# Kernel tuning notes

Hardware: AMD Instinct MI355X
Metric: run time of the kernel (lower is better)

The kernel has to match this reference:

```python
import jax, jax.numpy as jnp
import numpy as np

N, K, VF, FILT, H = 100000, 10, 128, 64, 3


def setup_inputs() -> dict:
    key = jax.random.key(0)
    ks = jax.random.split(key, 16)
    scale_w = float(np.sqrt(2.0 / VF))
    scale_a = float(np.sqrt(2.0 / (2 * FILT)))

    def pad_idx(k1, k2):
        idx = jax.random.randint(k1, (N, K), 0, N, dtype=jnp.int32)
        drop = jax.random.uniform(k2, (N, K)) < 0.2
        return jnp.where(drop, jnp.int32(-1), idx)

    return {
        "vertices_int": jax.random.normal(ks[0], (N, VF), jnp.float32),
        "vertices_nh": jax.random.normal(ks[1], (N, VF), jnp.float32),
        "nh_indices": pad_idx(ks[2], ks[3]),
        "int_indices": pad_idx(ks[4], ks[5]),
        "nh_edges": jax.random.uniform(ks[6], (N, K), jnp.float32),
        "int_edges": jax.random.uniform(ks[7], (N, K), jnp.float32),
        "is_int": jax.random.randint(ks[8], (N, 1), 0, 2, dtype=jnp.int32),
        "Wvc_int": jax.random.normal(ks[9], (H, VF, FILT), jnp.float32) * scale_w,
        "Wvc_nh": jax.random.normal(ks[10], (H, VF, FILT), jnp.float32) * scale_w,
        "Wvn_int": jax.random.normal(ks[11], (H, VF, FILT), jnp.float32) * scale_w,
        "Wvn_nh": jax.random.normal(ks[12], (H, VF, FILT), jnp.float32) * scale_w,
        "bv_int": jnp.zeros((H, FILT), jnp.float32),
        "bv_nh": jnp.zeros((H, FILT), jnp.float32),
        "a_int": jax.random.normal(ks[13], (H, 2 * FILT, 1), jnp.float32) * scale_a,
        "a_nh": jax.random.normal(ks[14], (H, 2 * FILT, 1), jnp.float32) * scale_a,
    }


def _gat_branch(v, idx, edges, Wvc, Wvn, a, bv):
    # v: [N,VF]; idx,edges: [N,K]; Wvc/Wvn: [H,VF,F]; a: [H,2F,1]; bv: [H,F]
    F_ = Wvc.shape[-1]
    Zc = jnp.einsum('nf,hfo->hno', v, Wvc)        # [H,N,F]
    Zn_src = jnp.einsum('nf,hfo->hno', v, Wvn)     # [H,N,F]
    gath = Zn_src[:, idx]                          # [H,N,K,F]  (-1 wraps, masked below)
    a1, a2 = a[:, :F_, 0], a[:, F_:, 0]            # [H,F] each
    part = (idx != -1).astype(v.dtype)             # [N,K]
    e = (jnp.einsum('hnkf,hf->hnk', gath, a1)
         + jnp.einsum('hnf,hf->hn', Zc, a2)[:, :, None]) * part * edges  # [H,N,K]
    alpha = jax.nn.softmax(e, axis=2)              # softmax over neighbor axis (torch dim=1)
    norm = jnp.maximum(part.sum(axis=1), 1.0)      # [N], zeros clamped to 1
    Zn = jnp.einsum('hnkf,hnk,nk->hnf', gath, alpha, part) / norm[None, :, None]
    z = jax.nn.relu(Zc + Zn + bv[:, None, :])      # [H,N,F]
    n = v.shape[0]
    return jnp.transpose(z, (1, 0, 2)).reshape(n, -1)  # concat heads -> [N, H*F]


def reference(vertices_int, vertices_nh, nh_indices, int_indices, nh_edges,
              int_edges, is_int, Wvc_int, Wvc_nh, Wvn_int, Wvn_nh,
              bv_int, bv_nh, a_int, a_nh):
    v_int = vertices_int * (is_int == 1).astype(vertices_int.dtype)
    v_nh = vertices_nh * (is_int == 0).astype(vertices_nh.dtype)
    out_int = _gat_branch(v_int, int_indices, int_edges, Wvc_int, Wvn_int, a_int, bv_int)
    out_nh = _gat_branch(v_nh, nh_indices, nh_edges, Wvc_nh, Wvn_nh, a_nh, bv_nh)
    return out_int, out_nh
```

## Files before the change

### kernel.cpp

```cpp
#include <hip/hip_runtime.h>


#define NN   100000
#define VFD  128
#define FILT 64
#define NH   3
#define KK   10
#define OUTC 192
#define NB   ((NN + 63) / 64)

typedef __attribute__((ext_vector_type(8))) short  short8;
typedef __attribute__((ext_vector_type(4))) float  f32x4;
typedef __attribute__((ext_vector_type(8))) __bf16 bf16x8;
typedef unsigned int u32;
typedef unsigned short u16;

static __device__ __forceinline__ f32x4 mfma_bf16(short8 a, short8 b, f32x4 c) {
    return __builtin_amdgcn_mfma_f32_16x16x32_bf16(
        __builtin_bit_cast(bf16x8, a), __builtin_bit_cast(bf16x8, b), c, 0, 0, 0);
}

static __device__ __forceinline__ void split2(float x, u16 &hi, u16 &lo) {
    u32 b = __float_as_uint(x);
    hi = (u16)(b >> 16);
    float hf = __uint_as_float(((u32)hi) << 16);
    lo = (u16)(__float_as_uint(x - hf) >> 16);
}

static __device__ __forceinline__ void gload16(const u32* g, u32* l) {
    __builtin_amdgcn_global_load_lds(
        (const __attribute__((address_space(1))) u32*)g,
        (__attribute__((address_space(3))) u32*)l, 16, 0, 0);
}

#define WT_CH_STRIDE   (2 * 8192)
#define WT_BR_STRIDE   (6 * WT_CH_STRIDE)
#define WA_OFF         (2 * WT_BR_STRIDE)
#define WA_BR_STRIDE   2048
#define PREP_WT_ELEMS  (2 * 6 * 8192)
#define PREP_WA_ELEMS  (2 * 16 * VFD)

__global__ void gat_prep(
    const float* __restrict__ Wvc_i, const float* __restrict__ Wvn_i,
    const float* __restrict__ Wvc_n, const float* __restrict__ Wvn_n,
    const float* __restrict__ a_i,  const float* __restrict__ a_n,
    u16* __restrict__ wsu)
{
    int t = blockIdx.x * blockDim.x + threadIdx.x;
    if (t < PREP_WT_ELEMS) {
        int b  = t / (6 * 8192);
        int r  = t % (6 * 8192);
        int ch = r / 8192;
        int e  = r % 8192;
        int f = e >> 6, col = e & 63;
        int m = ch / 3, h = ch % 3;
        const float* W = b ? (m ? Wvn_n : Wvc_n) : (m ? Wvn_i : Wvc_i);
        float val = W[h * (VFD * FILT) + f * FILT + col];
        u16 hi, lo; split2(val, hi, lo);
        int g    = f >> 3;
        int gran = g * 64 + (col ^ (g & 7));
        int idx  = gran * 8 + (f & 7);
        u16* dst = wsu + b * WT_BR_STRIDE + ch * WT_CH_STRIDE;
        dst[idx]        = hi;
        dst[8192 + idx] = lo;
    } else if (t < PREP_WT_ELEMS + PREP_WA_ELEMS) {
        int r = t - PREP_WT_ELEMS;
        int b = r / 2048, e = r % 2048;
        int col = e >> 7, f = e & 127;
        const float* a  = b ? a_n  : a_i;
        const float* Wc = b ? Wvc_n : Wvc_i;
        const float* Wn = b ? Wvn_n : Wvn_i;
        float val = 0.f;
        if (col < 3) {
            const float* wr = Wc + col * (VFD * FILT) + f * FILT;
            const float* av = a  + col * (2 * FILT) + FILT;
            for (int o = 0; o < FILT; ++o) val += wr[o] * av[o];
        } else if (col < 6) {
            int h = col - 3;
            const float* wr = Wn + h * (VFD * FILT) + f * FILT;
            const float* av = a  + h * (2 * FILT);
            for (int o = 0; o < FILT; ++o) val += wr[o] * av[o];
        }
        int idx = ((f >> 3) * 16 + col) * 8 + (f & 7);
        wsu[WA_OFF + b * WA_BR_STRIDE + idx] = (u16)(__float_as_uint(val) >> 16);
    }
}

__global__ __launch_bounds__(256, 2) void gat_pass1(
    const float* __restrict__ vert, const int* __restrict__ is_int, int want,
    const u16* __restrict__ wt_ws, const u16* __restrict__ wa_ws,
    float* __restrict__ zc_out, float* __restrict__ zn_src,
    float* __restrict__ s1, float* __restrict__ c2)
{
    __shared__ __align__(16) u16 vt_hi[8192];
    __shared__ __align__(16) u16 vt_lo[8192];
    __shared__ __align__(16) u16 wt[2 * 8192];
    __shared__ __align__(16) u16 wa[2048];

    const int tid  = threadIdx.x;
    const int row0 = blockIdx.x * 64;
    const int w    = tid >> 6;
    const int lane = tid & 63;
    const int rw = w >> 1, cw = w & 1;
    const int l15 = lane & 15, l4 = lane >> 4;

#pragma unroll
    for (int i = 0; i < 8; ++i) {
        int idx4 = i * 256 + tid;
        int row = idx4 >> 5, f4 = idx4 & 31;
        int n = row0 + row;
        float4 val = make_float4(0.f, 0.f, 0.f, 0.f);
        if (n < NN && is_int[n] == want)
            val = *reinterpret_cast<const float4*>(vert + (size_t)n * VFD + f4 * 4);
        u16 h0,h1,h2,h3, q0,q1,q2,q3;
        split2(val.x, h0, q0); split2(val.y, h1, q1);
        split2(val.z, h2, q2); split2(val.w, h3, q3);
        int g    = f4 >> 1;
        int gran = g * 64 + (row ^ (g & 7));
        int uidx = gran * 8 + (f4 & 1) * 4;
        uint2 hv = make_uint2((u32)h0 | ((u32)h1 << 16), (u32)h2 | ((u32)h3 << 16));
        uint2 lv = make_uint2((u32)q0 | ((u32)q1 << 16), (u32)q2 | ((u32)q3 << 16));
        *reinterpret_cast<uint2*>(vt_hi + uidx) = hv;
        *reinterpret_cast<uint2*>(vt_lo + uidx) = lv;
    }
    gload16((const u32*)(wa_ws + tid * 8), (u32*)(wa + tid * 8));

    for (int ch = 0; ch < 6; ++ch) {
        __syncthreads();
        const u16* src = wt_ws + ch * WT_CH_STRIDE;
#pragma unroll
        for (int j = 0; j < 8; ++j) {
            int cblk = j * 256 + tid;
            gload16((const u32*)(src + cblk * 8), (u32*)(wt + cblk * 8));
        }
        __syncthreads();

        const int m = ch / 3, h = ch % 3;
        f32x4 zero = {0.f, 0.f, 0.f, 0.f};
        f32x4 acc[2][2] = {{zero, zero}, {zero, zero}};

#pragma unroll
        for (int ks = 0; ks < 4; ++ks) {
            const int g = ks * 4 + l4;
            short8 ahi[2], alo[2], bhi[2], blo[2];
#pragma unroll
            for (int ti = 0; ti < 2; ++ti) {
                int row  = (rw * 2 + ti) * 16 + l15;
                int gran = g * 64 + (row ^ (g & 7));
                ahi[ti] = *reinterpret_cast<const short8*>(vt_hi + gran * 8);
                alo[ti] = *reinterpret_cast<const short8*>(vt_lo + gran * 8);
            }
#pragma unroll
            for (int tj = 0; tj < 2; ++tj) {
                int col  = (cw * 2 + tj) * 16 + l15;
                int gran = g * 64 + (col ^ (g & 7));
                bhi[tj] = *reinterpret_cast<const short8*>(wt + gran * 8);
                blo[tj] = *reinterpret_cast<const short8*>(wt + 8192 + gran * 8);
            }
#pragma unroll
            for (int ti = 0; ti < 2; ++ti)
#pragma unroll
                for (int tj = 0; tj < 2; ++tj) {
                    acc[ti][tj] = mfma_bf16(ahi[ti], bhi[tj], acc[ti][tj]);
                    acc[ti][tj] = mfma_bf16(ahi[ti], blo[tj], acc[ti][tj]);
                    acc[ti][tj] = mfma_bf16(alo[ti], bhi[tj], acc[ti][tj]);
                }
        }

        float* target = (m == 0) ? zc_out : zn_src;
#pragma unroll
        for (int ti = 0; ti < 2; ++ti)
#pragma unroll
            for (int tj = 0; tj < 2; ++tj) {
                int col = (cw * 2 + tj) * 16 + l15;
#pragma unroll
                for (int j = 0; j < 4; ++j) {
                    int n = row0 + (rw * 2 + ti) * 16 + l4 * 4 + j;
                    if (n < NN) target[(size_t)n * OUTC + h * FILT + col] = acc[ti][tj][j];
                }
            }
    }

    {
        f32x4 zero = {0.f, 0.f, 0.f, 0.f};
        f32x4 accS[2] = {zero, zero};
#pragma unroll
        for (int ks = 0; ks < 4; ++ks) {
            const int g = ks * 4 + l4;
            short8 wf = *reinterpret_cast<const short8*>(wa + (g * 16 + l15) * 8);
#pragma unroll
            for (int ti = 0; ti < 2; ++ti) {
                int row  = (rw * 2 + ti) * 16 + l15;
                int gran = g * 64 + (row ^ (g & 7));
                short8 ahi = *reinterpret_cast<const short8*>(vt_hi + gran * 8);
                short8 alo = *reinterpret_cast<const short8*>(vt_lo + gran * 8);
                accS[ti] = mfma_bf16(ahi, wf, accS[ti]);
                accS[ti] = mfma_bf16(alo, wf, accS[ti]);
            }
        }
        if (cw == 0 && l15 < 6) {
#pragma unroll
            for (int ti = 0; ti < 2; ++ti)
#pragma unroll
                for (int j = 0; j < 4; ++j) {
                    int n = row0 + (rw * 2 + ti) * 16 + l4 * 4 + j;
                    if (n < NN) {
                        float v = accS[ti][j];
                        if (l15 < 3) c2[l15 * NN + n] = v;
                        else         s1[(l15 - 3) * NN + n] = v;
                    }
                }
        }
    }
}

__global__ __launch_bounds__(256) void gat_pass2(
    const int* __restrict__ nidx, const float* __restrict__ edges,
    const float* __restrict__ zn_src, const float* __restrict__ s1,
    const float* __restrict__ c2, const float* __restrict__ bv,
    float* __restrict__ out)
{
    const int lane = threadIdx.x & 63;
    const int n    = (int)((blockIdx.x * blockDim.x + threadIdx.x) >> 6);
    if (n >= NN) return;

    int id[KK]; float ed[KK]; int sa[KK];
#pragma unroll
    for (int k = 0; k < KK; ++k) {
        id[k] = nidx[n * KK + k];
        ed[k] = edges[n * KK + k];
        sa[k] = max(id[k], 0);
    }

    float g[NH][KK];
#pragma unroll
    for (int k = 0; k < KK; ++k) {
        const float* rowp = zn_src + (size_t)sa[k] * OUTC + lane;
#pragma unroll
        for (int h = 0; h < NH; ++h) g[h][k] = rowp[h * FILT];
    }

    float npart = 0.f;
#pragma unroll
    for (int k = 0; k < KK; ++k) npart += (id[k] >= 0) ? 1.f : 0.f;
    const float rnorm = 1.f / fmaxf(npart, 1.f);

    float zacc[NH];
#pragma unroll
    for (int h = 0; h < NH; ++h) {
        const float c2v = c2[h * NN + n];
        float e[KK];
#pragma unroll
        for (int k = 0; k < KK; ++k) {
            float ev = (s1[h * NN + sa[k]] + c2v) * ed[k];
            e[k] = (id[k] >= 0) ? ev : 0.f;
        }
        float mx = e[0];
#pragma unroll
        for (int k = 1; k < KK; ++k) mx = fmaxf(mx, e[k]);
        float den = 0.f; float wk[KK];
#pragma unroll
        for (int k = 0; k < KK; ++k) { wk[k] = __expf(e[k] - mx); den += wk[k]; }
        const float scale = rnorm / den;
        float acc = 0.f;
#pragma unroll
        for (int k = 0; k < KK; ++k)
            acc = fmaf(g[h][k], (id[k] >= 0) ? wk[k] * scale : 0.f, acc);
        zacc[h] = acc;
    }

    float* orow = out + (size_t)n * OUTC;
#pragma unroll
    for (int h = 0; h < NH; ++h) {
        float res = orow[h * FILT + lane] + zacc[h] + bv[h * FILT + lane];
        orow[h * FILT + lane] = fmaxf(res, 0.f);
    }
}

extern "C" void kernel_launch(void* const* d_in, const int* in_sizes, int n_in,
                              void* d_out, int out_size, void* d_ws, size_t ws_size,
                              hipStream_t stream)
{
    const float* v_int  = (const float*)d_in[0];
    const float* v_nh   = (const float*)d_in[1];
    const int*   nh_idx = (const int*)d_in[2];
    const int*   in_idx = (const int*)d_in[3];
    const float* nh_e   = (const float*)d_in[4];
    const float* in_e   = (const float*)d_in[5];
    const int*   is_int = (const int*)d_in[6];
    const float* Wvc_i  = (const float*)d_in[7];
    const float* Wvc_n  = (const float*)d_in[8];
    const float* Wvn_i  = (const float*)d_in[9];
    const float* Wvn_n  = (const float*)d_in[10];
    const float* bv_i   = (const float*)d_in[11];
    const float* bv_n   = (const float*)d_in[12];
    const float* a_i    = (const float*)d_in[13];
    const float* a_n    = (const float*)d_in[14];

    float* out  = (float*)d_out;
    float* out2 = out + (size_t)NN * OUTC;

    float* zn_src = (float*)d_ws;
    float* s1     = zn_src + (size_t)NN * OUTC;
    float* c2     = s1 + (size_t)NH * NN;
    u16*   wsu    = (u16*)(c2 + (size_t)NH * NN);

    dim3 b(256);

    gat_prep<<<400, b, 0, stream>>>(Wvc_i, Wvn_i, Wvc_n, Wvn_n, a_i, a_n, wsu);

    gat_pass1<<<NB, b, 0, stream>>>(v_int, is_int, 1,
                                    wsu, wsu + WA_OFF,
                                    out, zn_src, s1, c2);
    gat_pass2<<<(NN * 64) / 256, b, 0, stream>>>(in_idx, in_e, zn_src, s1, c2, bv_i, out);

    gat_pass1<<<NB, b, 0, stream>>>(v_nh, is_int, 0,
                                    wsu + WT_BR_STRIDE, wsu + WA_OFF + WA_BR_STRIDE,
                                    out2, zn_src, s1, c2);
    gat_pass2<<<(NN * 64) / 256, b, 0, stream>>>(nh_idx, nh_e, zn_src, s1, c2, bv_n, out2);
}
```

Measured before the change: 584.1 us.

## Parallelize per-node softmax across lanes and vectorize neighbor gathers in pass2

Rewrites the second GAT pass so each wave spreads the (head, neighbor) attention logits across lanes, computing max and sum with xor shuffles instead of each lane redundantly evaluating all 30 logits. Neighbor feature rows are gathered with float4 loads by 48 lanes, and padded neighbors are skipped with a wave-uniform branch instead of loading row 0. This reduces redundant s1 loads and ALU work and lowers the gather traffic, at the cost of idle lanes (48 of 64 active in the gather phase) and shuffle overhead.

```diff
diff --git a/kernel.cpp b/kernel.cpp
--- a/kernel.cpp
+++ b/kernel.cpp
@@ -220,60 +220,69 @@
     const float* __restrict__ c2, const float* __restrict__ bv,
     float* __restrict__ out)
 {
-    const int lane = threadIdx.x & 63;
-    const int n    = (int)((blockIdx.x * blockDim.x + threadIdx.x) >> 6);
+    const int l = threadIdx.x & 63;
+    const int n = (int)((blockIdx.x * blockDim.x + threadIdx.x) >> 6);
     if (n >= NN) return;
 
-    int id[KK]; float ed[KK]; int sa[KK];
+    const int k16 = l & 15;
+    const int h   = l >> 4;
+    const int hc  = (h < 3) ? h : 2;
+
+    int   idv = -1;
+    float edv = 0.f;
+    if (l < KK) {
+        idv = nidx[n * KK + l];
+        edv = edges[n * KK + l];
+    }
+    const unsigned long long vm = __ballot(l < KK && idv >= 0);
+    const float rnorm = 1.f / fmaxf((float)__popcll(vm), 1.f);
+
+    const int   idb = __shfl(idv, k16);
+    const float edb = __shfl(edv, k16);
+    const int   sab = max(idb, 0);
+    const bool  kvalid = (k16 < KK);
+    const bool  evalid = kvalid && (idb >= 0);
+    const float c2v = c2[hc * NN + n];
+    const float s1v = s1[hc * NN + sab];
+    const float e   = evalid ? (s1v + c2v) * edb : 0.f;
+
+    float er = kvalid ? e : -3.4e38f;
+#pragma unroll
+    for (int m = 1; m < 16; m <<= 1) er = fmaxf(er, __shfl_xor(er, m));
+    const float wk = kvalid ? __expf(e - er) : 0.f;
+    float dn = wk;
+#pragma unroll
+    for (int m = 1; m < 16; m <<= 1) dn += __shfl_xor(dn, m);
+    const float wfin = evalid ? wk * (rnorm / dn) : 0.f;
+
+    const bool act = (l < 48);
+    float4 acc = make_float4(0.f, 0.f, 0.f, 0.f);
 #pragma unroll
     for (int k = 0; k < KK; ++k) {
-        id[k] = nidx[n * KK + k];
-        ed[k] = edges[n * KK + k];
-        sa[k] = max(id[k], 0);
-    }
-
-    float g[NH][KK];
-#pragma unroll
-    for (int k = 0; k < KK; ++k) {
-        const float* rowp = zn_src + (size_t)sa[k] * OUTC + lane;
-#pragma unroll
-        for (int h = 0; h < NH; ++h) g[h][k] = rowp[h * FILT];
-    }
-
-    float npart = 0.f;
-#pragma unroll
-    for (int k = 0; k < KK; ++k) npart += (id[k] >= 0) ? 1.f : 0.f;
-    const float rnorm = 1.f / fmaxf(npart, 1.f);
-
-    float zacc[NH];
-#pragma unroll
-    for (int h = 0; h < NH; ++h) {
-        const float c2v = c2[h * NN + n];
-        float e[KK];
-#pragma unroll
-        for (int k = 0; k < KK; ++k) {
-            float ev = (s1[h * NN + sa[k]] + c2v) * ed[k];
-            e[k] = (id[k] >= 0) ? ev : 0.f;
-        }
-        float mx = e[0];
-#pragma unroll
-        for (int k = 1; k < KK; ++k) mx = fmaxf(mx, e[k]);
-        float den = 0.f; float wk[KK];
-#pragma unroll
-        for (int k = 0; k < KK; ++k) { wk[k] = __expf(e[k] - mx); den += wk[k]; }
-        const float scale = rnorm / den;
-        float acc = 0.f;
-#pragma unroll
-        for (int k = 0; k < KK; ++k)
-            acc = fmaf(g[h][k], (id[k] >= 0) ? wk[k] * scale : 0.f, acc);
-        zacc[h] = acc;
-    }
-
-    float* orow = out + (size_t)n * OUTC;
-#pragma unroll
-    for (int h = 0; h < NH; ++h) {
-        float res = orow[h * FILT + lane] + zacc[h] + bv[h * FILT + lane];
-        orow[h * FILT + lane] = fmaxf(res, 0.f);
+        const int idk = __builtin_amdgcn_readlane(idv, k);
+        if (idk >= 0) {
+            const float wb = __shfl(wfin, k, 16);
+            if (act) {
+                const float4 g = *reinterpret_cast<const float4*>(
+                    zn_src + (size_t)idk * OUTC + l * 4);
+                acc.x = fmaf(g.x, wb, acc.x);
+                acc.y = fmaf(g.y, wb, acc.y);
+                acc.z = fmaf(g.z, wb, acc.z);
+                acc.w = fmaf(g.w, wb, acc.w);
+            }
+        }
+    }
+
+    if (act) {
+        float* op = out + (size_t)n * OUTC + l * 4;
+        const float4 zc = *reinterpret_cast<const float4*>(op);
+        const float4 bq = *reinterpret_cast<const float4*>(bv + l * 4);
+        float4 r;
+        r.x = fmaxf(zc.x + acc.x + bq.x, 0.f);
+        r.y = fmaxf(zc.y + acc.y + bq.y, 0.f);
+        r.z = fmaxf(zc.z + acc.z + bq.z, 0.f);
+        r.w = fmaxf(zc.w + acc.w + bq.w, 0.f);
+        *reinterpret_cast<float4*>(op) = r;
     }
 }
 
```

After: 581.9 us. No clear change (-0.4%).
